# Kernel optimization log

Hardware: AMD Instinct MI355X
Metric: run time of the kernel (lower is better)

## Reference

```python
import jax, jax.numpy as jnp
import numpy as np

N = 100000      # num_nodes
E = 1600000     # num_edges
D_IN = 256      # input_dim
H = 64          # hidden_dim
OUT = 32        # output_dim
EMB = 128       # node2vec embedding_dim
HEADS = 2       # GAT heads (concat=False -> mean over heads)
NEG_SLOPE = 0.2 # GATConv leaky_relu default


def setup_inputs() -> dict:
    key = jax.random.key(0)
    ks = jax.random.split(key, 24)
    s = lambda k, shape, fan: (jax.random.normal(k, shape, jnp.float32) * (1.0 / np.sqrt(fan)))
    return {
        "x": jax.random.normal(ks[0], (N, D_IN), jnp.float32),
        "edge_index": jax.random.randint(ks[1], (2, E), 0, N, jnp.int64),
        # frozen node2vec embedding table (used under no_grad in the original)
        "n2v_emb": jax.random.normal(ks[2], (N, EMB), jnp.float32),
        "n2v_proj_w": s(ks[3], (EMB, H), EMB), "n2v_proj_b": jnp.zeros((H,), jnp.float32),
        "input_proj_w": s(ks[4], (D_IN + H, H), D_IN + H), "input_proj_b": jnp.zeros((H,), jnp.float32),
        "gate_w": s(ks[5], (D_IN + H, H), D_IN + H), "gate_b": jnp.zeros((H,), jnp.float32),
        # SAGEConv layers: out = mean_agg(x_j) @ wl + bl + x @ wr
        "sage0_wl": s(ks[6], (H, H), H), "sage0_bl": jnp.zeros((H,), jnp.float32), "sage0_wr": s(ks[7], (H, H), H),
        "sage1_wl": s(ks[8], (H, H), H), "sage1_bl": jnp.zeros((H,), jnp.float32), "sage1_wr": s(ks[9], (H, H), H),
        # GATConv(H, H, heads=2, concat=False)
        "gat_w": s(ks[10], (H, HEADS * H), H),
        "gat_att_src": s(ks[11], (HEADS, H), H), "gat_att_dst": s(ks[12], (HEADS, H), H),
        "gat_b": jnp.zeros((H,), jnp.float32),
        "fin_wl": s(ks[13], (H, OUT), H), "fin_bl": jnp.zeros((OUT,), jnp.float32), "fin_wr": s(ks[14], (H, OUT), H),
    }


def _sage(h, src, dst, wl, bl, wr, n):
    # PyG SAGEConv with mean aggregation: lin_l(mean_j h_j) + lin_r(h_i)
    msum = jax.ops.segment_sum(h[src], dst, num_segments=n)
    deg = jax.ops.segment_sum(jnp.ones((src.shape[0],), h.dtype), dst, num_segments=n)
    agg = msum / jnp.maximum(deg, 1.0)[:, None]
    return agg @ wl + bl + h @ wr


def _gat(h, src, dst, w, att_src, att_dst, b, n):
    # GATConv with self-loops (PyG default), heads averaged (concat=False)
    loops = jnp.arange(n, dtype=src.dtype)
    src = jnp.concatenate([src, loops]); dst = jnp.concatenate([dst, loops])
    xh = (h @ w).reshape(n, HEADS, H)                     # [n, heads, H]
    a_src = jnp.einsum('nhd,hd->nh', xh, att_src)         # [n, heads]
    a_dst = jnp.einsum('nhd,hd->nh', xh, att_dst)
    e = jax.nn.leaky_relu(a_src[src] + a_dst[dst], NEG_SLOPE)  # [E', heads]
    emax = jax.ops.segment_max(e, dst, num_segments=n)
    ex = jnp.exp(e - emax[dst])
    esum = jax.ops.segment_sum(ex, dst, num_segments=n)
    alpha = ex / (esum[dst] + 1e-16)                      # edge softmax per dst, per head
    out = jax.ops.segment_sum(alpha[:, :, None] * xh[src], dst, num_segments=n)
    return out.mean(axis=1) + b                           # [n, H]


def reference(x, edge_index, n2v_emb, n2v_proj_w, n2v_proj_b, input_proj_w, input_proj_b,
              gate_w, gate_b, sage0_wl, sage0_bl, sage0_wr, sage1_wl, sage1_bl, sage1_wr,
              gat_w, gat_att_src, gat_att_dst, gat_b, fin_wl, fin_bl, fin_wr):
    n = x.shape[0]
    src, dst = edge_index[0], edge_index[1]
    # node2vec embeddings are frozen (torch.no_grad in original)
    n2v = jax.lax.stop_gradient(n2v_emb)
    n2v_p = n2v @ n2v_proj_w + n2v_proj_b                 # [n, H]
    combined = jnp.concatenate([x, n2v_p], axis=-1)       # [n, D_IN+H]
    gate = jax.nn.sigmoid(combined @ gate_w + gate_b)
    x_proj = combined @ input_proj_w + input_proj_b
    raw_proj = jnp.concatenate([x, jnp.zeros((n, H), x.dtype)], axis=-1) @ input_proj_w + input_proj_b
    h = gate * x_proj + (1.0 - gate) * raw_proj           # node_indices=None -> all nodes
    h = jax.nn.relu(_sage(h, src, dst, sage0_wl, sage0_bl, sage0_wr, n))
    h = jax.nn.relu(_sage(h, src, dst, sage1_wl, sage1_bl, sage1_wr, n))
    h = jax.nn.relu(_gat(h, src, dst, gat_w, gat_att_src, gat_att_dst, gat_b, n))
    return _sage(h, src, dst, fin_wl, fin_bl, fin_wr, n)  # [n, OUT]
```

## Files before the change

### kernel.cpp

```cpp
#include <hip/hip_runtime.h>
#include <math.h>

#define NN 100000
#define NE 1600000
#define DIN 256
#define HD 64
#define OUTD 32
#define EMBD 128
#define SLOPE 0.2f
#define AST 68
#define NT ((NN + 63) / 64)
#define SCHUNK 1024
#define SNBLK ((NN + SCHUNK - 1) / SCHUNK)
#define FCH 25000
#define FNC ((NE + FCH - 1) / FCH)
#define NFILL (8 * FNC)

typedef __attribute__((ext_vector_type(8))) short bf16x8;
typedef __attribute__((ext_vector_type(8))) unsigned short u16x8;
typedef __attribute__((ext_vector_type(4))) float f32x4;

__device__ __forceinline__ float lrelu(float x) { return x > 0.f ? x : SLOPE * x; }
__device__ __forceinline__ ushort f2b(float f) {
    unsigned u = __float_as_uint(f);
    return (ushort)((u + 0x7FFFu + ((u >> 16) & 1u)) >> 16);
}
__device__ __forceinline__ float b2f(ushort v) { return __uint_as_float(((unsigned)v) << 16); }

__global__ void k_count(const int* __restrict__ dst, int* __restrict__ cnt) {
    int i = blockIdx.x * blockDim.x + threadIdx.x;
    if (i < NE) atomicAdd(&cnt[dst[i]], 1);
}

__global__ __launch_bounds__(256) void k_scan1(const int* __restrict__ cnt,
                                               int* __restrict__ rowptr,
                                               int* __restrict__ blksum) {
    __shared__ int ts[256];
    int base = blockIdx.x * SCHUNK + threadIdx.x * 4;
    int v0 = 0, v1 = 0, v2 = 0, v3 = 0;
    if (base < NN)     v0 = cnt[base];
    if (base + 1 < NN) v1 = cnt[base + 1];
    if (base + 2 < NN) v2 = cnt[base + 2];
    if (base + 3 < NN) v3 = cnt[base + 3];
    int s = v0 + v1 + v2 + v3;
    ts[threadIdx.x] = s;
    __syncthreads();
    for (int off = 1; off < 256; off <<= 1) {
        int w = (threadIdx.x >= off) ? ts[threadIdx.x - off] : 0;
        __syncthreads();
        ts[threadIdx.x] += w;
        __syncthreads();
    }
    int excl = ts[threadIdx.x] - s;
    if (base < NN)     rowptr[base]     = excl;
    if (base + 1 < NN) rowptr[base + 1] = excl + v0;
    if (base + 2 < NN) rowptr[base + 2] = excl + v0 + v1;
    if (base + 3 < NN) rowptr[base + 3] = excl + v0 + v1 + v2;
    if (threadIdx.x == 255) blksum[blockIdx.x] = ts[255];
}

__global__ __launch_bounds__(128) void k_scan2(int* __restrict__ blksum) {
    __shared__ int ts[128];
    int t = threadIdx.x;
    int v = (t < SNBLK) ? blksum[t] : 0;
    ts[t] = v;
    __syncthreads();
    for (int off = 1; off < 128; off <<= 1) {
        int w = (t >= off) ? ts[t - off] : 0;
        __syncthreads();
        ts[t] += w;
        __syncthreads();
    }
    if (t < SNBLK) blksum[t] = ts[t] - v;
}

__global__ void k_scan3(const int* __restrict__ blksum, const int* __restrict__ cnt,
                        int* __restrict__ rowptr, int* __restrict__ cursor,
                        float* __restrict__ invdeg) {
    int i = blockIdx.x * blockDim.x + threadIdx.x;
    if (i < NN) {
        int v = rowptr[i] + blksum[i >> 10];
        rowptr[i] = v;
        cursor[i] = v;
        invdeg[i] = 1.0f / fmaxf((float)cnt[i], 1.0f);
    }
    if (i == 0) rowptr[NN] = NE;
}

__device__ __forceinline__ void stageA(const float* __restrict__ g, int nbase, int ldg, int koff,
                                       float (*As)[AST]) {
    for (int i = threadIdx.x; i < 1024; i += 256) {
        int m = i >> 4, k4 = (i & 15) << 2;
        int row = nbase + m;
        if (row >= NN) row = NN - 1;
        *(float4*)&As[m][k4] = *(const float4*)&g[(size_t)row * ldg + koff + k4];
    }
}
__device__ __forceinline__ void stageAb(const ushort* __restrict__ g, int nbase, int ldg,
                                        float (*As)[AST]) {
    for (int i = threadIdx.x; i < 1024; i += 256) {
        int m = i >> 4, k4 = (i & 15) << 2;
        int row = nbase + m;
        if (row >= NN) row = NN - 1;
        ushort4 v = *(const ushort4*)&g[(size_t)row * ldg + k4];
        As[m][k4] = b2f(v.x); As[m][k4 + 1] = b2f(v.y);
        As[m][k4 + 2] = b2f(v.z); As[m][k4 + 3] = b2f(v.w);
    }
}
__device__ __forceinline__ void stageW(const float* __restrict__ g, float* Ws) {
    for (int i = threadIdx.x; i < 1024; i += 256) ((float4*)Ws)[i] = ((const float4*)g)[i];
}
__device__ __forceinline__ void stageWcols(const float* __restrict__ g, int ldg, int coff,
                                           float* Ws) {
    for (int i = threadIdx.x; i < 1024; i += 256) {
        int r = i >> 4, c4 = (i & 15) << 2;
        *(float4*)&Ws[r * 64 + c4] = *(const float4*)&g[r * ldg + coff + c4];
    }
}
__device__ __forceinline__ void mac16v(const float (*As)[AST], const float* __restrict__ Ws,
                                       float (*acc)[4], int tr, int tc) {
#pragma unroll 4
    for (int k4 = 0; k4 < 64; k4 += 4) {
        float4 a0 = *(const float4*)&As[tr * 4 + 0][k4];
        float4 a1 = *(const float4*)&As[tr * 4 + 1][k4];
        float4 a2 = *(const float4*)&As[tr * 4 + 2][k4];
        float4 a3 = *(const float4*)&As[tr * 4 + 3][k4];
#pragma unroll
        for (int j = 0; j < 4; j++) {
            float4 w = *(const float4*)&Ws[(k4 + j) * 64 + tc * 4];
            float e0 = (&a0.x)[j], e1 = (&a1.x)[j], e2 = (&a2.x)[j], e3 = (&a3.x)[j];
            acc[0][0] += e0 * w.x; acc[0][1] += e0 * w.y; acc[0][2] += e0 * w.z; acc[0][3] += e0 * w.w;
            acc[1][0] += e1 * w.x; acc[1][1] += e1 * w.y; acc[1][2] += e1 * w.z; acc[1][3] += e1 * w.w;
            acc[2][0] += e2 * w.x; acc[2][1] += e2 * w.y; acc[2][2] += e2 * w.z; acc[2][3] += e2 * w.w;
            acc[3][0] += e3 * w.x; acc[3][1] += e3 * w.y; acc[3][2] += e3 * w.z; acc[3][3] += e3 * w.w;
        }
    }
}

__global__ __launch_bounds__(256) void k_megafront(
        const float* __restrict__ x, const float* __restrict__ n2v,
        const float* __restrict__ n2v_w, const float* __restrict__ n2v_b,
        const float* __restrict__ ip_w, const float* __restrict__ ip_b,
        const float* __restrict__ gate_w, const float* __restrict__ gate_b,
        float* __restrict__ h0, ushort* __restrict__ h0b,
        const int* __restrict__ esrc, const int* __restrict__ edst,
        int* __restrict__ cursor, int* __restrict__ colsrc) {
    __shared__ ushort Ah[64][40], Al[64][40];
    __shared__ ushort Bih[64][40], Bil[64][40];
    __shared__ ushort Bgh[64][40], Bgl[64][40];

    if (blockIdx.x < NFILL) {
        int cls = blockIdx.x & 7;
        int chunk = blockIdx.x >> 3;
        int lo = cls * (NN / 8);
        int hi = (cls == 7) ? NN : lo + (NN / 8);
        int beg = chunk * FCH;
        int end = min(beg + FCH, NE);
        for (int i = beg + (int)threadIdx.x; i < end; i += 256) {
            int d = edst[i];
            if (d >= lo && d < hi) {
                int pos = atomicAdd(&cursor[d], 1);
                colsrc[pos] = esrc[i];
            }
        }
        return;
    }

    int nbase = (blockIdx.x - NFILL) * 64;
    int tid = threadIdx.x;
    int w = tid >> 6, l = tid & 63;
    int lr = l & 15, lg = l >> 4, lk = lg * 8;
    f32x4 zero = {0.f, 0.f, 0.f, 0.f};
    f32x4 araw[4], ag[4], adel[4], pn[4];
#pragma unroll
    for (int t = 0; t < 4; t++) { araw[t] = zero; ag[t] = zero; adel[t] = zero; pn[t] = zero; }

    int arow = tid >> 2, ak0 = (tid & 3) << 3;
    int garow = nbase + arow;
    if (garow >= NN) garow = NN - 1;

    for (int c = 0; c < 4; c++) {
        if (c) __syncthreads();
        {
            const float* ap = &n2v[(size_t)garow * EMBD + c * 32 + ak0];
            u16x8 th, tl;
#pragma unroll
            for (int u = 0; u < 8; u++) {
                float v = ap[u];
                ushort h = f2b(v);
                th[u] = h;
                tl[u] = f2b(v - b2f(h));
            }
            *(u16x8*)&Ah[arow][ak0] = th;
            *(u16x8*)&Al[arow][ak0] = tl;
        }
        {
            const float* pw = &n2v_w[(size_t)(c * 32 + w * 8) * 64 + l];
            u16x8 ih, il;
#pragma unroll
            for (int u = 0; u < 8; u++) {
                float v = pw[u * 64];
                ushort h = f2b(v);
                ih[u] = h;
                il[u] = f2b(v - b2f(h));
            }
            *(u16x8*)&Bih[l][w * 8] = ih;
            *(u16x8*)&Bil[l][w * 8] = il;
        }
        __syncthreads();
        bf16x8 ah = *(const bf16x8*)&Ah[w * 16 + lr][lk];
        bf16x8 al = *(const bf16x8*)&Al[w * 16 + lr][lk];
#pragma unroll
        for (int t = 0; t < 4; t++) {
            int col = t * 16 + lr;
            bf16x8 bih = *(const bf16x8*)&Bih[col][lk];
            bf16x8 bil = *(const bf16x8*)&Bil[col][lk];
            f32x4 r = pn[t];
            r = __builtin_amdgcn_mfma_f32_16x16x32_bf16(ah, bih, r, 0, 0, 0);
            r = __builtin_amdgcn_mfma_f32_16x16x32_bf16(ah, bil, r, 0, 0, 0);
            r = __builtin_amdgcn_mfma_f32_16x16x32_bf16(al, bih, r, 0, 0, 0);
            pn[t] = r;
        }
    }
#pragma unroll
    for (int t = 0; t < 4; t++) {
        float nb = n2v_b[t * 16 + lr];
#pragma unroll
        for (int r = 0; r < 4; r++) pn[t][r] += nb;
    }

    for (int c = 0; c < 8; c++) {
        __syncthreads();
        {
            const float* ap = &x[(size_t)garow * DIN + c * 32 + ak0];
            u16x8 th, tl;
#pragma unroll
            for (int u = 0; u < 8; u++) {
                float v = ap[u];
                ushort h = f2b(v);
                th[u] = h;
                tl[u] = f2b(v - b2f(h));
            }
            *(u16x8*)&Ah[arow][ak0] = th;
            *(u16x8*)&Al[arow][ak0] = tl;
        }
        {
            const float* pi = &ip_w[(size_t)(c * 32 + w * 8) * 64 + l];
            const float* pg = &gate_w[(size_t)(c * 32 + w * 8) * 64 + l];
            u16x8 ih, il, gh, gl2;
#pragma unroll
            for (int u = 0; u < 8; u++) {
                float v = pi[u * 64];
                ushort h = f2b(v);
                ih[u] = h; il[u] = f2b(v - b2f(h));
                float g = pg[u * 64];
                ushort hg = f2b(g);
                gh[u] = hg; gl2[u] = f2b(g - b2f(hg));
            }
            *(u16x8*)&Bih[l][w * 8] = ih;
            *(u16x8*)&Bil[l][w * 8] = il;
            *(u16x8*)&Bgh[l][w * 8] = gh;
            *(u16x8*)&Bgl[l][w * 8] = gl2;
        }
        __syncthreads();
        bf16x8 ah = *(const bf16x8*)&Ah[w * 16 + lr][lk];
        bf16x8 al = *(const bf16x8*)&Al[w * 16 + lr][lk];
#pragma unroll
        for (int t = 0; t < 4; t++) {
            int col = t * 16 + lr;
            bf16x8 bih = *(const bf16x8*)&Bih[col][lk];
            bf16x8 bil = *(const bf16x8*)&Bil[col][lk];
            bf16x8 bgh = *(const bf16x8*)&Bgh[col][lk];
            bf16x8 bgl = *(const bf16x8*)&Bgl[col][lk];
            f32x4 r = araw[t];
            r = __builtin_amdgcn_mfma_f32_16x16x32_bf16(ah, bih, r, 0, 0, 0);
            r = __builtin_amdgcn_mfma_f32_16x16x32_bf16(ah, bil, r, 0, 0, 0);
            r = __builtin_amdgcn_mfma_f32_16x16x32_bf16(al, bih, r, 0, 0, 0);
            araw[t] = r;
            f32x4 g = ag[t];
            g = __builtin_amdgcn_mfma_f32_16x16x32_bf16(ah, bgh, g, 0, 0, 0);
            g = __builtin_amdgcn_mfma_f32_16x16x32_bf16(ah, bgl, g, 0, 0, 0);
            g = __builtin_amdgcn_mfma_f32_16x16x32_bf16(al, bgh, g, 0, 0, 0);
            ag[t] = g;
        }
    }

    for (int c = 0; c < 2; c++) {
        __syncthreads();
#pragma unroll
        for (int tt = 0; tt < 2; tt++) {
            int t = c * 2 + tt;
            int ak = tt * 16 + lr;
#pragma unroll
            for (int r = 0; r < 4; r++) {
                int row = w * 16 + lg * 4 + r;
                float v = pn[t][r];
                ushort h = f2b(v);
                Ah[row][ak] = h;
                Al[row][ak] = f2b(v - b2f(h));
            }
        }
        {
            const float* pi = &ip_w[(size_t)(DIN + c * 32 + w * 8) * 64 + l];
            const float* pg = &gate_w[(size_t)(DIN + c * 32 + w * 8) * 64 + l];
            u16x8 ih, il, gh, gl2;
#pragma unroll
            for (int u = 0; u < 8; u++) {
                float v = pi[u * 64];
                ushort h = f2b(v);
                ih[u] = h; il[u] = f2b(v - b2f(h));
                float g = pg[u * 64];
                ushort hg = f2b(g);
                gh[u] = hg; gl2[u] = f2b(g - b2f(hg));
            }
            *(u16x8*)&Bih[l][w * 8] = ih;
            *(u16x8*)&Bil[l][w * 8] = il;
            *(u16x8*)&Bgh[l][w * 8] = gh;
            *(u16x8*)&Bgl[l][w * 8] = gl2;
        }
        __syncthreads();
        bf16x8 ah = *(const bf16x8*)&Ah[w * 16 + lr][lk];
        bf16x8 al = *(const bf16x8*)&Al[w * 16 + lr][lk];
#pragma unroll
        for (int t = 0; t < 4; t++) {
            int col = t * 16 + lr;
            bf16x8 bih = *(const bf16x8*)&Bih[col][lk];
            bf16x8 bil = *(const bf16x8*)&Bil[col][lk];
            bf16x8 bgh = *(const bf16x8*)&Bgh[col][lk];
            bf16x8 bgl = *(const bf16x8*)&Bgl[col][lk];
            f32x4 r = adel[t];
            r = __builtin_amdgcn_mfma_f32_16x16x32_bf16(ah, bih, r, 0, 0, 0);
            r = __builtin_amdgcn_mfma_f32_16x16x32_bf16(ah, bil, r, 0, 0, 0);
            r = __builtin_amdgcn_mfma_f32_16x16x32_bf16(al, bih, r, 0, 0, 0);
            adel[t] = r;
            f32x4 g = ag[t];
            g = __builtin_amdgcn_mfma_f32_16x16x32_bf16(ah, bgh, g, 0, 0, 0);
            g = __builtin_amdgcn_mfma_f32_16x16x32_bf16(ah, bgl, g, 0, 0, 0);
            g = __builtin_amdgcn_mfma_f32_16x16x32_bf16(al, bgh, g, 0, 0, 0);
            ag[t] = g;
        }
    }
#pragma unroll
    for (int t = 0; t < 4; t++) {
        int col = t * 16 + lr;
        float ib = ip_b[col], gb2 = gate_b[col];
#pragma unroll
        for (int r = 0; r < 4; r++) {
            int row = nbase + w * 16 + lg * 4 + r;
            if (row < NN) {
                float raw = araw[t][r] + ib;
                float sg = 1.f / (1.f + __expf(-(ag[t][r] + gb2)));
                float o = raw + sg * adel[t][r];
                h0[(size_t)row * HD + col] = o;
                h0b[(size_t)row * HD + col] = f2b(o);
            }
        }
    }
}

__global__ void k_gather_mean(const int* __restrict__ rowptr, const int* __restrict__ colsrc,
                              const float* __restrict__ invdeg, const ushort* __restrict__ hb,
                              ushort* __restrict__ aggb) {
    int t = threadIdx.x & 63;
    int lane16 = t & 15, quarter = t >> 4;
    int gw = blockIdx.x * (blockDim.x >> 6) + (threadIdx.x >> 6);
    int stride = gridDim.x * (blockDim.x >> 6);
    for (int n = gw; n < NN; n += stride) {
        int bg = rowptr[n], en = rowptr[n + 1];
        float a0 = 0.f, a1 = 0.f, a2 = 0.f, a3 = 0.f;
        int i = bg + quarter;
        for (; i + 4 < en; i += 8) {
            int sa = colsrc[i], sb = colsrc[i + 4];
            ushort4 va = *(const ushort4*)&hb[(size_t)sa * HD + lane16 * 4];
            ushort4 vb = *(const ushort4*)&hb[(size_t)sb * HD + lane16 * 4];
            a0 += b2f(va.x) + b2f(vb.x);
            a1 += b2f(va.y) + b2f(vb.y);
            a2 += b2f(va.z) + b2f(vb.z);
            a3 += b2f(va.w) + b2f(vb.w);
        }
        for (; i < en; i += 4) {
            int s = colsrc[i];
            ushort4 v = *(const ushort4*)&hb[(size_t)s * HD + lane16 * 4];
            a0 += b2f(v.x);
            a1 += b2f(v.y);
            a2 += b2f(v.z);
            a3 += b2f(v.w);
        }
        a0 += __shfl_xor(a0, 32); a1 += __shfl_xor(a1, 32);
        a2 += __shfl_xor(a2, 32); a3 += __shfl_xor(a3, 32);
        a0 += __shfl_xor(a0, 16); a1 += __shfl_xor(a1, 16);
        a2 += __shfl_xor(a2, 16); a3 += __shfl_xor(a3, 16);
        if (quarter == 0) {
            float id = invdeg[n];
            ushort4 o = {f2b(a0 * id), f2b(a1 * id), f2b(a2 * id), f2b(a3 * id)};
            *(ushort4*)&aggb[(size_t)n * HD + lane16 * 4] = o;
        }
    }
}

__global__ __launch_bounds__(256) void k_sage_t(const ushort* __restrict__ aggb,
                                                const float* __restrict__ h,
                                                const float* __restrict__ wl,
                                                const float* __restrict__ bl,
                                                const float* __restrict__ wr,
                                                float* __restrict__ hout,
                                                ushort* __restrict__ houtb) {
    __shared__ float As[64][AST];
    __shared__ float Ws[64 * 64];
    int nbase = blockIdx.x * 64;
    int tc = threadIdx.x & 15, tr = threadIdx.x >> 4;
    float acc[4][4] = {};
    stageAb(aggb, nbase, HD, As);
    stageW(wl, Ws);
    __syncthreads();
    mac16v(As, Ws, acc, tr, tc);
    __syncthreads();
    stageA(h, nbase, HD, 0, As);
    stageW(wr, Ws);
    __syncthreads();
    mac16v(As, Ws, acc, tr, tc);
    float b0 = bl[tc * 4], b1 = bl[tc * 4 + 1], b2 = bl[tc * 4 + 2], b3 = bl[tc * 4 + 3];
#pragma unroll
    for (int i = 0; i < 4; i++) {
        int row = nbase + tr * 4 + i;
        if (row < NN) {
            float4 o = {fmaxf(acc[i][0] + b0, 0.f), fmaxf(acc[i][1] + b1, 0.f),
                        fmaxf(acc[i][2] + b2, 0.f), fmaxf(acc[i][3] + b3, 0.f)};
            *(float4*)&hout[(size_t)row * HD + tc * 4] = o;
            ushort4 ob = {f2b(o.x), f2b(o.y), f2b(o.z), f2b(o.w)};
            *(ushort4*)&houtb[(size_t)row * HD + tc * 4] = ob;
        }
    }
}

__global__ __launch_bounds__(256) void k_gatxh_t(const float* __restrict__ h,
                                                 const float* __restrict__ w,
                                                 const float* __restrict__ att_s,
                                                 const float* __restrict__ att_d,
                                                 ushort* __restrict__ xhb,
                                                 float* __restrict__ a_s,
                                                 float* __restrict__ a_d) {
    __shared__ float As[64][AST];
    __shared__ float Ws[64 * 64];
    int nbase = blockIdx.x * 64;
    int tc = threadIdx.x & 15, tr = threadIdx.x >> 4;
    stageA(h, nbase, HD, 0, As);
#pragma unroll
    for (int half = 0; half < 2; half++) {
        if (half) __syncthreads();
        stageWcols(w, 128, half * 64, Ws);
        __syncthreads();
        float acc[4][4] = {};
        mac16v(As, Ws, acc, tr, tc);
        float as0 = att_s[half * 64 + tc * 4], as1 = att_s[half * 64 + tc * 4 + 1];
        float as2 = att_s[half * 64 + tc * 4 + 2], as3 = att_s[half * 64 + tc * 4 + 3];
        float ad0 = att_d[half * 64 + tc * 4], ad1 = att_d[half * 64 + tc * 4 + 1];
        float ad2 = att_d[half * 64 + tc * 4 + 2], ad3 = att_d[half * 64 + tc * 4 + 3];
#pragma unroll
        for (int i = 0; i < 4; i++) {
            int row = nbase + tr * 4 + i;
            float ps = acc[i][0] * as0 + acc[i][1] * as1 + acc[i][2] * as2 + acc[i][3] * as3;
            float pd = acc[i][0] * ad0 + acc[i][1] * ad1 + acc[i][2] * ad2 + acc[i][3] * ad3;
#pragma unroll
            for (int off = 8; off; off >>= 1) {
                ps += __shfl_xor(ps, off);
                pd += __shfl_xor(pd, off);
            }
            if (row < NN) {
                ushort4 ob = {f2b(acc[i][0]), f2b(acc[i][1]), f2b(acc[i][2]), f2b(acc[i][3])};
                *(ushort4*)&xhb[(size_t)row * 128 + half * 64 + tc * 4] = ob;
                if (tc == 0) {
                    a_s[row * 2 + half] = ps;
                    a_d[row * 2 + half] = pd;
                }
            }
        }
    }
}

__global__ void k_gat_fused(const int* __restrict__ rowptr, const int* __restrict__ colsrc,
                            const float* __restrict__ a_s, const float* __restrict__ a_d,
                            const ushort* __restrict__ xhb, const float* __restrict__ gb,
                            float* __restrict__ hout) {
    int t = threadIdx.x & 63;
    int lane = t & 31, half = t >> 5;
    int bl4 = (lane & 15) * 4;
    float4 bias4 = *(const float4*)&gb[bl4];
    int gw = blockIdx.x * (blockDim.x >> 6) + (threadIdx.x >> 6);
    int stride = gridDim.x * (blockDim.x >> 6);
    for (int n = gw; n < NN; n += stride) {
        int bg = rowptr[n], en = rowptr[n + 1];
        float ad0 = a_d[n * 2], ad1 = a_d[n * 2 + 1];
        float a0 = 0.f, a1 = 0.f, a2 = 0.f, a3 = 0.f;
        float ss0 = 0.f, ss1 = 0.f;
        int i = bg + half;
        for (; i + 6 < en; i += 8) {
            int sa = colsrc[i], sb = colsrc[i + 2], sc = colsrc[i + 4], sd = colsrc[i + 6];
            float2 ava = *(const float2*)&a_s[sa * 2];
            float2 avb = *(const float2*)&a_s[sb * 2];
            float2 avc = *(const float2*)&a_s[sc * 2];
            float2 avd = *(const float2*)&a_s[sd * 2];
            ushort4 xva = *(const ushort4*)&xhb[(size_t)sa * 128 + lane * 4];
            ushort4 xvb = *(const ushort4*)&xhb[(size_t)sb * 128 + lane * 4];
            ushort4 xvc = *(const ushort4*)&xhb[(size_t)sc * 128 + lane * 4];
            ushort4 xvd = *(const ushort4*)&xhb[(size_t)sd * 128 + lane * 4];
            float wa0 = __expf(lrelu(ava.x + ad0)), wa1 = __expf(lrelu(ava.y + ad1));
            float wb0 = __expf(lrelu(avb.x + ad0)), wb1 = __expf(lrelu(avb.y + ad1));
            float wc0 = __expf(lrelu(avc.x + ad0)), wc1 = __expf(lrelu(avc.y + ad1));
            float wd0 = __expf(lrelu(avd.x + ad0)), wd1 = __expf(lrelu(avd.y + ad1));
            ss0 += wa0 + wb0 + wc0 + wd0;
            ss1 += wa1 + wb1 + wc1 + wd1;
            float wsa = (lane < 16) ? wa0 : wa1;
            float wsb = (lane < 16) ? wb0 : wb1;
            float wsc = (lane < 16) ? wc0 : wc1;
            float wsd = (lane < 16) ? wd0 : wd1;
            a0 += wsa * b2f(xva.x) + wsb * b2f(xvb.x) + wsc * b2f(xvc.x) + wsd * b2f(xvd.x);
            a1 += wsa * b2f(xva.y) + wsb * b2f(xvb.y) + wsc * b2f(xvc.y) + wsd * b2f(xvd.y);
            a2 += wsa * b2f(xva.z) + wsb * b2f(xvb.z) + wsc * b2f(xvc.z) + wsd * b2f(xvd.z);
            a3 += wsa * b2f(xva.w) + wsb * b2f(xvb.w) + wsc * b2f(xvc.w) + wsd * b2f(xvd.w);
        }
        for (; i < en; i += 2) {
            int s = colsrc[i];
            float2 av = *(const float2*)&a_s[s * 2];
            float w0 = __expf(lrelu(av.x + ad0));
            float w1 = __expf(lrelu(av.y + ad1));
            ss0 += w0;
            ss1 += w1;
            float wsel = (lane < 16) ? w0 : w1;
            ushort4 xv = *(const ushort4*)&xhb[(size_t)s * 128 + lane * 4];
            a0 += wsel * b2f(xv.x);
            a1 += wsel * b2f(xv.y);
            a2 += wsel * b2f(xv.z);
            a3 += wsel * b2f(xv.w);
        }
        if (half == 0) {
            float2 av = *(const float2*)&a_s[n * 2];
            float w0 = __expf(lrelu(av.x + ad0));
            float w1 = __expf(lrelu(av.y + ad1));
            ss0 += w0;
            ss1 += w1;
            float wsel = (lane < 16) ? w0 : w1;
            ushort4 xv = *(const ushort4*)&xhb[(size_t)n * 128 + lane * 4];
            a0 += wsel * b2f(xv.x);
            a1 += wsel * b2f(xv.y);
            a2 += wsel * b2f(xv.z);
            a3 += wsel * b2f(xv.w);
        }
        ss0 += __shfl_xor(ss0, 32);
        ss1 += __shfl_xor(ss1, 32);
        a0 += __shfl_xor(a0, 32);
        a1 += __shfl_xor(a1, 32);
        a2 += __shfl_xor(a2, 32);
        a3 += __shfl_xor(a3, 32);
        float r = (lane < 16) ? (0.5f / (ss0 + 1e-16f)) : (0.5f / (ss1 + 1e-16f));
        float v0 = a0 * r, v1 = a1 * r, v2 = a2 * r, v3 = a3 * r;
        float p0 = __shfl_xor(v0, 16);
        float p1 = __shfl_xor(v1, 16);
        float p2 = __shfl_xor(v2, 16);
        float p3 = __shfl_xor(v3, 16);
        if (half == 0 && lane < 16) {
            float4 o = {fmaxf(v0 + p0 + bias4.x, 0.f), fmaxf(v1 + p1 + bias4.y, 0.f),
                        fmaxf(v2 + p2 + bias4.z, 0.f), fmaxf(v3 + p3 + bias4.w, 0.f)};
            *(float4*)&hout[(size_t)n * HD + lane * 4] = o;
        }
    }
}

__global__ void k_pfin(const float* __restrict__ h, const float* __restrict__ wl,
                       ushort* __restrict__ Pb) {
    __shared__ float sw[HD * OUTD];
    for (int i = threadIdx.x; i < HD * OUTD; i += blockDim.x) sw[i] = wl[i];
    __syncthreads();
    int t = threadIdx.x & 63;
    int c = t & 31, half = t >> 5;
    int gw = blockIdx.x * (blockDim.x >> 6) + (threadIdx.x >> 6);
    int stride = gridDim.x * (blockDim.x >> 6);
    for (int n = gw; n < NN; n += stride) {
        float hv = h[(size_t)n * HD + t];
        float acc = 0.f;
#pragma unroll 8
        for (int i = 0; i < 32; i++) {
            float bb = __shfl(hv, half * 32 + i);
            acc += bb * sw[half * 1024 + i * 32 + c];
        }
        acc += __shfl_xor(acc, 32);
        if (half == 0) Pb[(size_t)n * OUTD + c] = f2b(acc);
    }
}

__global__ void k_final_fused(const int* __restrict__ rowptr, const int* __restrict__ colsrc,
                              const float* __restrict__ invdeg, const ushort* __restrict__ Pb,
                              const float* __restrict__ h, const float* __restrict__ bl,
                              const float* __restrict__ wr, float* __restrict__ out) {
    __shared__ float sw[HD * OUTD];
    for (int i = threadIdx.x; i < HD * OUTD; i += blockDim.x) sw[i] = wr[i];
    __syncthreads();
    int t = threadIdx.x & 63;
    int j = t & 31, half = t >> 5;
    int quarter = t >> 4, lane16 = t & 15;
    float bias = bl[j];
    int gw = blockIdx.x * (blockDim.x >> 6) + (threadIdx.x >> 6);
    int stride = gridDim.x * (blockDim.x >> 6);
    for (int n = gw; n < NN; n += stride) {
        int bg = rowptr[n], en = rowptr[n + 1];
        float a0 = 0.f, a1 = 0.f;
        int i = bg + quarter;
        for (; i + 4 < en; i += 8) {
            int sa = colsrc[i], sb = colsrc[i + 4];
            ushort2 va = *(const ushort2*)&Pb[(size_t)sa * OUTD + lane16 * 2];
            ushort2 vb = *(const ushort2*)&Pb[(size_t)sb * OUTD + lane16 * 2];
            a0 += b2f(va.x) + b2f(vb.x);
            a1 += b2f(va.y) + b2f(vb.y);
        }
        for (; i < en; i += 4) {
            int s = colsrc[i];
            ushort2 v = *(const ushort2*)&Pb[(size_t)s * OUTD + lane16 * 2];
            a0 += b2f(v.x);
            a1 += b2f(v.y);
        }
        a0 += __shfl_xor(a0, 32);
        a1 += __shfl_xor(a1, 32);
        a0 += __shfl_xor(a0, 16);
        a1 += __shfl_xor(a1, 16);
        float hv = h[(size_t)n * HD + t];
        float o = 0.f;
#pragma unroll 8
        for (int i2 = 0; i2 < 32; i2++) {
            float bb = __shfl(hv, half * 32 + i2);
            o += bb * sw[half * 1024 + i2 * 32 + j];
        }
        o += __shfl_xor(o, 32);
        float ga = __shfl(a0, j >> 1);
        float gb_ = __shfl(a1, j >> 1);
        float gv = (j & 1) ? gb_ : ga;
        if (half == 0) out[(size_t)n * OUTD + j] = gv * invdeg[n] + bias + o;
    }
}

extern "C" void kernel_launch(void* const* d_in, const int* in_sizes, int n_in,
                              void* d_out, int out_size, void* d_ws, size_t ws_size,
                              hipStream_t stream) {
    const float* x      = (const float*)d_in[0];
    const int*   eidx   = (const int*)d_in[1];
    const float* n2v    = (const float*)d_in[2];
    const float* n2v_w  = (const float*)d_in[3];
    const float* n2v_b  = (const float*)d_in[4];
    const float* ip_w   = (const float*)d_in[5];
    const float* ip_b   = (const float*)d_in[6];
    const float* gate_w = (const float*)d_in[7];
    const float* gate_b = (const float*)d_in[8];
    const float* s0_wl  = (const float*)d_in[9];
    const float* s0_bl  = (const float*)d_in[10];
    const float* s0_wr  = (const float*)d_in[11];
    const float* s1_wl  = (const float*)d_in[12];
    const float* s1_bl  = (const float*)d_in[13];
    const float* s1_wr  = (const float*)d_in[14];
    const float* gat_w  = (const float*)d_in[15];
    const float* att_s  = (const float*)d_in[16];
    const float* att_d  = (const float*)d_in[17];
    const float* gat_b  = (const float*)d_in[18];
    const float* f_wl   = (const float*)d_in[19];
    const float* f_bl   = (const float*)d_in[20];
    const float* f_wr   = (const float*)d_in[21];

    const int* src = eidx;
    const int* dst = eidx + NE;

    float*  ws     = (float*)d_ws;
    float*  invdeg = ws;
    float*  S1     = invdeg + NN;
    float*  S2     = S1 + (size_t)NN * HD;
    ushort* aggb   = (ushort*)(S2 + (size_t)NN * HD);
    float*  a_s    = (float*)(aggb + (size_t)NN * HD);
    float*  a_d    = a_s + (size_t)NN * 2;
    ushort* Pb     = (ushort*)(a_d + (size_t)NN * 2);
    ushort* hb     = Pb + (size_t)NN * OUTD;
    ushort* xhb    = hb + (size_t)NN * HD;
    int*    cnt    = (int*)(xhb + (size_t)NN * 128);
    int*    rowptr = cnt + NN;
    int*    cursor = rowptr + NN + 1;
    int*    blksum = cursor + NN;
    int*    colsrc = blksum + 128;

    float* out = (float*)d_out;

    const int BT = 256;
    dim3 b128(128), b256(BT);
    int eblk = (NE + BT - 1) / BT;
    int nblk = (NN + BT - 1) / BT;

    hipMemsetAsync(cnt, 0, (size_t)NN * 4, stream);
    k_count<<<eblk, b256, 0, stream>>>(dst, cnt);
    k_scan1<<<SNBLK, b256, 0, stream>>>(cnt, rowptr, blksum);
    k_scan2<<<1, b128, 0, stream>>>(blksum);
    k_scan3<<<nblk, b256, 0, stream>>>(blksum, cnt, rowptr, cursor, invdeg);

    k_megafront<<<NFILL + NT, b256, 0, stream>>>(x, n2v, n2v_w, n2v_b, ip_w, ip_b,
                                                 gate_w, gate_b, S2, hb,
                                                 src, dst, cursor, colsrc);

    k_gather_mean<<<2048, b256, 0, stream>>>(rowptr, colsrc, invdeg, hb, aggb);
    k_sage_t<<<NT, b256, 0, stream>>>(aggb, S2, s0_wl, s0_bl, s0_wr, S1, hb);

    k_gather_mean<<<2048, b256, 0, stream>>>(rowptr, colsrc, invdeg, hb, aggb);
    k_sage_t<<<NT, b256, 0, stream>>>(aggb, S1, s1_wl, s1_bl, s1_wr, S2, hb);

    k_gatxh_t<<<NT, b256, 0, stream>>>(S2, gat_w, att_s, att_d, xhb, a_s, a_d);
    k_gat_fused<<<2048, b256, 0, stream>>>(rowptr, colsrc, a_s, a_d, xhb, gat_b, S1);

    k_pfin<<<2048, b256, 0, stream>>>(S1, f_wl, Pb);
    k_final_fused<<<2048, b256, 0, stream>>>(rowptr, colsrc, invdeg, Pb, S1, f_bl, f_wr, out);
}
```

Baseline: 648.1 us.

## Fuse neighbor mean-gather into SAGE GEMM tiles and fold GAT projection into layer 1

The standalone gather-mean kernels are removed. Each 64-node SAGE tile block now gathers its neighbors' bf16 features straight into shared memory before the dense transforms, which removes the aggregated-feature round trip through global memory and several launches. The second SAGE layer's ReLU output stays in shared memory and feeds the GAT linear/attention projection in the same kernel, so its fp32 output is never written back. The cost is a less parallel gather: 4 nodes per 16-lane group, sequential per node, over only NT blocks with high shared-memory use. Load imbalance from degree variance and lower memory-level parallelism may hurt.

After: 746.3 us. +15.2%, slower.

```diff
diff --git a/kernel.cpp b/kernel.cpp
--- a/kernel.cpp
+++ b/kernel.cpp
@@ -96,17 +96,6 @@
         *(float4*)&As[m][k4] = *(const float4*)&g[(size_t)row * ldg + koff + k4];
     }
 }
-__device__ __forceinline__ void stageAb(const ushort* __restrict__ g, int nbase, int ldg,
-                                        float (*As)[AST]) {
-    for (int i = threadIdx.x; i < 1024; i += 256) {
-        int m = i >> 4, k4 = (i & 15) << 2;
-        int row = nbase + m;
-        if (row >= NN) row = NN - 1;
-        ushort4 v = *(const ushort4*)&g[(size_t)row * ldg + k4];
-        As[m][k4] = b2f(v.x); As[m][k4 + 1] = b2f(v.y);
-        As[m][k4 + 2] = b2f(v.z); As[m][k4 + 3] = b2f(v.w);
-    }
-}
 __device__ __forceinline__ void stageW(const float* __restrict__ g, float* Ws) {
     for (int i = threadIdx.x; i < 1024; i += 256) ((float4*)Ws)[i] = ((const float4*)g)[i];
 }
@@ -134,6 +123,46 @@
             acc[2][0] += e2 * w.x; acc[2][1] += e2 * w.y; acc[2][2] += e2 * w.z; acc[2][3] += e2 * w.w;
             acc[3][0] += e3 * w.x; acc[3][1] += e3 * w.y; acc[3][2] += e3 * w.z; acc[3][3] += e3 * w.w;
         }
+    }
+}
+
+__device__ __forceinline__ void gatherA(const int* __restrict__ rowptr,
+                                        const int* __restrict__ colsrc,
+                                        const float* __restrict__ invdeg,
+                                        const ushort* __restrict__ hbin,
+                                        int nbase, float (*As)[AST]) {
+    int t = threadIdx.x;
+    int lane16 = t & 15, quarter = t >> 4;
+#pragma unroll
+    for (int j = 0; j < 4; j++) {
+        int ln = quarter + j * 16;
+        int n = nbase + ln;
+        int nn = (n < NN) ? n : NN - 1;
+        int bg = rowptr[nn], en = rowptr[nn + 1];
+        float a0 = 0.f, a1 = 0.f, a2 = 0.f, a3 = 0.f;
+        int i = bg;
+        for (; i + 1 < en; i += 2) {
+            int sa = colsrc[i], sb = colsrc[i + 1];
+            ushort4 va = *(const ushort4*)&hbin[(size_t)sa * HD + lane16 * 4];
+            ushort4 vb = *(const ushort4*)&hbin[(size_t)sb * HD + lane16 * 4];
+            a0 += b2f(va.x) + b2f(vb.x);
+            a1 += b2f(va.y) + b2f(vb.y);
+            a2 += b2f(va.z) + b2f(vb.z);
+            a3 += b2f(va.w) + b2f(vb.w);
+        }
+        for (; i < en; i++) {
+            int s = colsrc[i];
+            ushort4 v = *(const ushort4*)&hbin[(size_t)s * HD + lane16 * 4];
+            a0 += b2f(v.x);
+            a1 += b2f(v.y);
+            a2 += b2f(v.z);
+            a3 += b2f(v.w);
+        }
+        float id = invdeg[nn];
+        As[ln][lane16 * 4 + 0] = a0 * id;
+        As[ln][lane16 * 4 + 1] = a1 * id;
+        As[ln][lane16 * 4 + 2] = a2 * id;
+        As[ln][lane16 * 4 + 3] = a3 * id;
     }
 }
 
@@ -358,64 +387,23 @@
     }
 }
 
-__global__ void k_gather_mean(const int* __restrict__ rowptr, const int* __restrict__ colsrc,
-                              const float* __restrict__ invdeg, const ushort* __restrict__ hb,
-                              ushort* __restrict__ aggb) {
-    int t = threadIdx.x & 63;
-    int lane16 = t & 15, quarter = t >> 4;
-    int gw = blockIdx.x * (blockDim.x >> 6) + (threadIdx.x >> 6);
-    int stride = gridDim.x * (blockDim.x >> 6);
-    for (int n = gw; n < NN; n += stride) {
-        int bg = rowptr[n], en = rowptr[n + 1];
-        float a0 = 0.f, a1 = 0.f, a2 = 0.f, a3 = 0.f;
-        int i = bg + quarter;
-        for (; i + 4 < en; i += 8) {
-            int sa = colsrc[i], sb = colsrc[i + 4];
-            ushort4 va = *(const ushort4*)&hb[(size_t)sa * HD + lane16 * 4];
-            ushort4 vb = *(const ushort4*)&hb[(size_t)sb * HD + lane16 * 4];
-            a0 += b2f(va.x) + b2f(vb.x);
-            a1 += b2f(va.y) + b2f(vb.y);
-            a2 += b2f(va.z) + b2f(vb.z);
-            a3 += b2f(va.w) + b2f(vb.w);
-        }
-        for (; i < en; i += 4) {
-            int s = colsrc[i];
-            ushort4 v = *(const ushort4*)&hb[(size_t)s * HD + lane16 * 4];
-            a0 += b2f(v.x);
-            a1 += b2f(v.y);
-            a2 += b2f(v.z);
-            a3 += b2f(v.w);
-        }
-        a0 += __shfl_xor(a0, 32); a1 += __shfl_xor(a1, 32);
-        a2 += __shfl_xor(a2, 32); a3 += __shfl_xor(a3, 32);
-        a0 += __shfl_xor(a0, 16); a1 += __shfl_xor(a1, 16);
-        a2 += __shfl_xor(a2, 16); a3 += __shfl_xor(a3, 16);
-        if (quarter == 0) {
-            float id = invdeg[n];
-            ushort4 o = {f2b(a0 * id), f2b(a1 * id), f2b(a2 * id), f2b(a3 * id)};
-            *(ushort4*)&aggb[(size_t)n * HD + lane16 * 4] = o;
-        }
-    }
-}
-
-__global__ __launch_bounds__(256) void k_sage_t(const ushort* __restrict__ aggb,
-                                                const float* __restrict__ h,
-                                                const float* __restrict__ wl,
-                                                const float* __restrict__ bl,
-                                                const float* __restrict__ wr,
-                                                float* __restrict__ hout,
-                                                ushort* __restrict__ houtb) {
+__global__ __launch_bounds__(256) void k_sage0_full(
+        const int* __restrict__ rowptr, const int* __restrict__ colsrc,
+        const float* __restrict__ invdeg, const ushort* __restrict__ hbin,
+        const float* __restrict__ hfp, const float* __restrict__ wl,
+        const float* __restrict__ bl, const float* __restrict__ wr,
+        float* __restrict__ hout, ushort* __restrict__ hbout) {
     __shared__ float As[64][AST];
     __shared__ float Ws[64 * 64];
     int nbase = blockIdx.x * 64;
     int tc = threadIdx.x & 15, tr = threadIdx.x >> 4;
+    stageW(wl, Ws);
+    gatherA(rowptr, colsrc, invdeg, hbin, nbase, As);
+    __syncthreads();
     float acc[4][4] = {};
-    stageAb(aggb, nbase, HD, As);
-    stageW(wl, Ws);
-    __syncthreads();
     mac16v(As, Ws, acc, tr, tc);
     __syncthreads();
-    stageA(h, nbase, HD, 0, As);
+    stageA(hfp, nbase, HD, 0, As);
     stageW(wr, Ws);
     __syncthreads();
     mac16v(As, Ws, acc, tr, tc);
@@ -428,30 +416,51 @@
                         fmaxf(acc[i][2] + b2, 0.f), fmaxf(acc[i][3] + b3, 0.f)};
             *(float4*)&hout[(size_t)row * HD + tc * 4] = o;
             ushort4 ob = {f2b(o.x), f2b(o.y), f2b(o.z), f2b(o.w)};
-            *(ushort4*)&houtb[(size_t)row * HD + tc * 4] = ob;
-        }
-    }
-}
-
-__global__ __launch_bounds__(256) void k_gatxh_t(const float* __restrict__ h,
-                                                 const float* __restrict__ w,
-                                                 const float* __restrict__ att_s,
-                                                 const float* __restrict__ att_d,
-                                                 ushort* __restrict__ xhb,
-                                                 float* __restrict__ a_s,
-                                                 float* __restrict__ a_d) {
+            *(ushort4*)&hbout[(size_t)row * HD + tc * 4] = ob;
+        }
+    }
+}
+
+__global__ __launch_bounds__(256) void k_sage1gat_full(
+        const int* __restrict__ rowptr, const int* __restrict__ colsrc,
+        const float* __restrict__ invdeg, const ushort* __restrict__ hbin,
+        const float* __restrict__ hfp, const float* __restrict__ wl,
+        const float* __restrict__ bl, const float* __restrict__ wr,
+        const float* __restrict__ gat_w, const float* __restrict__ att_s,
+        const float* __restrict__ att_d, ushort* __restrict__ xhb,
+        float* __restrict__ a_s, float* __restrict__ a_d) {
     __shared__ float As[64][AST];
     __shared__ float Ws[64 * 64];
     int nbase = blockIdx.x * 64;
     int tc = threadIdx.x & 15, tr = threadIdx.x >> 4;
-    stageA(h, nbase, HD, 0, As);
+    stageW(wl, Ws);
+    gatherA(rowptr, colsrc, invdeg, hbin, nbase, As);
+    __syncthreads();
+    float acc[4][4] = {};
+    mac16v(As, Ws, acc, tr, tc);
+    __syncthreads();
+    stageA(hfp, nbase, HD, 0, As);
+    stageW(wr, Ws);
+    __syncthreads();
+    mac16v(As, Ws, acc, tr, tc);
+    __syncthreads();
+    {
+        float b0 = bl[tc * 4], b1 = bl[tc * 4 + 1], b2 = bl[tc * 4 + 2], b3 = bl[tc * 4 + 3];
+#pragma unroll
+        for (int i = 0; i < 4; i++) {
+            As[tr * 4 + i][tc * 4 + 0] = fmaxf(acc[i][0] + b0, 0.f);
+            As[tr * 4 + i][tc * 4 + 1] = fmaxf(acc[i][1] + b1, 0.f);
+            As[tr * 4 + i][tc * 4 + 2] = fmaxf(acc[i][2] + b2, 0.f);
+            As[tr * 4 + i][tc * 4 + 3] = fmaxf(acc[i][3] + b3, 0.f);
+        }
+    }
 #pragma unroll
     for (int half = 0; half < 2; half++) {
-        if (half) __syncthreads();
-        stageWcols(w, 128, half * 64, Ws);
-        __syncthreads();
-        float acc[4][4] = {};
-        mac16v(As, Ws, acc, tr, tc);
+        __syncthreads();
+        stageWcols(gat_w, 128, half * 64, Ws);
+        __syncthreads();
+        float acc2[4][4] = {};
+        mac16v(As, Ws, acc2, tr, tc);
         float as0 = att_s[half * 64 + tc * 4], as1 = att_s[half * 64 + tc * 4 + 1];
         float as2 = att_s[half * 64 + tc * 4 + 2], as3 = att_s[half * 64 + tc * 4 + 3];
         float ad0 = att_d[half * 64 + tc * 4], ad1 = att_d[half * 64 + tc * 4 + 1];
@@ -459,15 +468,15 @@
 #pragma unroll
         for (int i = 0; i < 4; i++) {
             int row = nbase + tr * 4 + i;
-            float ps = acc[i][0] * as0 + acc[i][1] * as1 + acc[i][2] * as2 + acc[i][3] * as3;
-            float pd = acc[i][0] * ad0 + acc[i][1] * ad1 + acc[i][2] * ad2 + acc[i][3] * ad3;
+            float ps = acc2[i][0] * as0 + acc2[i][1] * as1 + acc2[i][2] * as2 + acc2[i][3] * as3;
+            float pd = acc2[i][0] * ad0 + acc2[i][1] * ad1 + acc2[i][2] * ad2 + acc2[i][3] * ad3;
 #pragma unroll
             for (int off = 8; off; off >>= 1) {
                 ps += __shfl_xor(ps, off);
                 pd += __shfl_xor(pd, off);
             }
             if (row < NN) {
-                ushort4 ob = {f2b(acc[i][0]), f2b(acc[i][1]), f2b(acc[i][2]), f2b(acc[i][3])};
+                ushort4 ob = {f2b(acc2[i][0]), f2b(acc2[i][1]), f2b(acc2[i][2]), f2b(acc2[i][3])};
                 *(ushort4*)&xhb[(size_t)row * 128 + half * 64 + tc * 4] = ob;
                 if (tc == 0) {
                     a_s[row * 2 + half] = ps;
@@ -670,8 +679,8 @@
     float*  invdeg = ws;
     float*  S1     = invdeg + NN;
     float*  S2     = S1 + (size_t)NN * HD;
-    ushort* aggb   = (ushort*)(S2 + (size_t)NN * HD);
-    float*  a_s    = (float*)(aggb + (size_t)NN * HD);
+    ushort* hb1    = (ushort*)(S2 + (size_t)NN * HD);
+    float*  a_s    = (float*)(hb1 + (size_t)NN * HD);
     float*  a_d    = a_s + (size_t)NN * 2;
     ushort* Pb     = (ushort*)(a_d + (size_t)NN * 2);
     ushort* hb     = Pb + (size_t)NN * OUTD;
@@ -699,15 +708,15 @@
                                                  gate_w, gate_b, S2, hb,
                                                  src, dst, cursor, colsrc);
 
-    k_gather_mean<<<2048, b256, 0, stream>>>(rowptr, colsrc, invdeg, hb, aggb);
-    k_sage_t<<<NT, b256, 0, stream>>>(aggb, S2, s0_wl, s0_bl, s0_wr, S1, hb);
-
-    k_gather_mean<<<2048, b256, 0, stream>>>(rowptr, colsrc, invdeg, hb, aggb);
-    k_sage_t<<<NT, b256, 0, stream>>>(aggb, S1, s1_wl, s1_bl, s1_wr, S2, hb);
-
-    k_gatxh_t<<<NT, b256, 0, stream>>>(S2, gat_w, att_s, att_d, xhb, a_s, a_d);
-    k_gat_fused<<<2048, b256, 0, stream>>>(rowptr, colsrc, a_s, a_d, xhb, gat_b, S1);
-
-    k_pfin<<<2048, b256, 0, stream>>>(S1, f_wl, Pb);
-    k_final_fused<<<2048, b256, 0, stream>>>(rowptr, colsrc, invdeg, Pb, S1, f_bl, f_wr, out);
-}
+    k_sage0_full<<<NT, b256, 0, stream>>>(rowptr, colsrc, invdeg, hb, S2,
+                                          s0_wl, s0_bl, s0_wr, S1, hb1);
+
+    k_sage1gat_full<<<NT, b256, 0, stream>>>(rowptr, colsrc, invdeg, hb1, S1,
+                                             s1_wl, s1_bl, s1_wr,
+                                             gat_w, att_s, att_d, xhb, a_s, a_d);
+
+    k_gat_fused<<<2048, b256, 0, stream>>>(rowptr, colsrc, a_s, a_d, xhb, gat_b, S2);
+
+    k_pfin<<<2048, b256, 0, stream>>>(S2, f_wl, Pb);
+    k_final_fused<<<2048, b256, 0, stream>>>(rowptr, colsrc, invdeg, Pb, S2, f_bl, f_wr, out);
+}
```
